# Optimization experiments

Hardware: AMD Instinct MI355X
Metric: run time of the kernel (lower is better)

The kernel has to match this reference:

```python
import jax, jax.numpy as jnp
from jax import lax
import numpy as np

T = 480000
LAYER = 32
N_HIDDEN = 2  # num_layers - 1
C1 = 4.7e-9


def _lin_init(key, out_dim, in_dim):
    kw, kb = jax.random.split(key)
    bound = 1.0 / np.sqrt(in_dim)
    W = jax.random.uniform(kw, (out_dim, in_dim), jnp.float32, -bound, bound)
    b = jax.random.uniform(kb, (out_dim,), jnp.float32, -bound, bound)
    return W, b


def setup_inputs() -> dict:
    key = jax.random.key(0)
    ks = jax.random.split(key, 8)
    v_in = jax.random.normal(ks[0], (T,), jnp.float32)
    vs_r = 10000.0 * (0.9 + 0.2 * jax.random.uniform(ks[1], (T,), jnp.float32))
    fs = jnp.full((T,), 48000.0, jnp.float32)
    W_in, b_in = _lin_init(ks[2], LAYER, 2)
    Wh, bh = [], []
    for i in range(N_HIDDEN):
        W, b = _lin_init(ks[3 + i], LAYER, LAYER)
        Wh.append(W)
        bh.append(b)
    W_h = jnp.stack(Wh)   # [N_HIDDEN, LAYER, LAYER]
    b_h = jnp.stack(bh)   # [N_HIDDEN, LAYER]
    W_out, b_out = _lin_init(ks[6], 1, LAYER)
    return {"v_in": v_in, "vs_r": vs_r, "fs": fs,
            "W_in": W_in, "b_in": b_in, "W_h": W_h, "b_h": b_h,
            "W_out": W_out, "b_out": b_out}


def reference(v_in, vs_r, fs, W_in, b_in, W_h, b_h, W_out, b_out):
    # --- per-timestep WDF port parameters (vectorized precompute) ---
    c1_r = 1.0 / (2.0 * C1 * fs)                      # [T]
    r0 = c1_r * vs_r / (c1_r + vs_r)                  # [T]
    p1_r = jnp.stack([r0, c1_r, vs_r], axis=-1)       # [T,3]
    p1_g = 1.0 / p1_r                                 # [T,3]
    P = 2.0 * p1_g / jnp.sum(p1_g, axis=-1, keepdims=True)  # [T,3]
    row0 = P.at[:, 0].add(-1.0)                       # p1[0,:] per step
    row1 = P.at[:, 1].add(-1.0)                       # p1[1,:] per step
    dp_r = r0 / 3000.0                                # [T]

    def mlp(x):  # x: [2] -> scalar, DiodePair(num_layers=3, layer_size=32)
        h = jax.nn.relu(W_in @ x + b_in)
        for i in range(W_h.shape[0]):
            h = jax.nn.relu(W_h[i] @ h + b_h[i])
        return (W_out @ h + b_out)[0]

    def step(carry, inp):
        a0, b1 = carry          # prev dp_b, prev p1_b[1]
        v, r0t, r1t, drt = inp
        a = jnp.stack([a0, b1, v])         # p1_a after updates [1],[2]
        dp_a = r0t @ a                      # p1_b[0]
        dp_b = mlp(jnp.stack([dp_a, drt]))
        a2 = jnp.stack([dp_b, b1, v])      # p1_a with [0] = dp_b
        b1n = r1t @ a2                      # p1_b[1]
        return (dp_b, b1n), 0.5 * (dp_a + dp_b)

    z = jnp.zeros((), jnp.float32)
    _, out = lax.scan(step, (z, z), (v_in, row0, row1, dp_r))
    return out
```

## Files before the change

kernel.cpp:

```cpp
#include <hip/hip_runtime.h>
#include <hip/hip_bf16.h>

#define C1_CONST 4.7e-9f
#define CHUNK 5
#define WARM  10
#define CPW   32

typedef _Float16 f16;
typedef unsigned int u32;
typedef f16   f16x8  __attribute__((ext_vector_type(8)));
typedef u32   u32x4  __attribute__((ext_vector_type(4)));
typedef float f32x16 __attribute__((ext_vector_type(16)));

#define MFMA(A, B, C) __builtin_amdgcn_mfma_f32_32x32x16_f16((A), (B), (C), 0, 0, 0)

__device__ __forceinline__ u32 packp(float x0, float x1) {
    return __builtin_bit_cast(u32, __builtin_amdgcn_cvt_pkrtz(x0, x1));
}

__global__ __launch_bounds__(64, 2) void scan_kernel(
    const float* __restrict__ v_in, const float* __restrict__ vs_r,
    const float* __restrict__ fs,
    const float* __restrict__ W_in, const float* __restrict__ b_in,
    const float* __restrict__ W_h,  const float* __restrict__ b_h,
    const float* __restrict__ W_out, const float* __restrict__ b_out,
    float* __restrict__ out, int T) {
    const int lane = threadIdx.x & 63;
    const int c    = lane & 31;
    const int h    = lane >> 5;
    const int xaddr = (lane ^ 32) << 2;

    auto xr32 = [&](float v) {
        return __int_as_float(__builtin_amdgcn_ds_bpermute(xaddr, __float_as_int(v)));
    };

    f16x8 AA0, AA1, AB0, AB1;
#pragma unroll
    for (int jj = 0; jj < 8; ++jj) {
        int k0 = (jj & 3) + 4 * h + 8 * (jj >> 2);
        int k1 = k0 + 16;
        AA0[jj] = (f16)W_h[c * 32 + k0];
        AA1[jj] = (f16)W_h[c * 32 + k1];
        AB0[jj] = (f16)W_h[1024 + c * 32 + k0];
        AB1[jj] = (f16)W_h[1024 + c * 32 + k1];
    }

    f32x16 bAf, bBf;
    float wo_r[16];
#pragma unroll
    for (int r = 0; r < 16; ++r) {
        int row = (r & 3) + 8 * (r >> 2) + 4 * h;
        bAf[r] = b_h[row];
        bBf[r] = b_h[32 + row];
        wo_r[r] = W_out[row];
    }
    const float bo = b_out[0];

    float wi0c[16], wi1c[16], bic[16];
#pragma unroll
    for (int s = 0; s < 2; ++s)
#pragma unroll
        for (int jj = 0; jj < 8; ++jj) {
            int k = (jj & 3) + 4 * h + 8 * (jj >> 2) + 16 * s;
            wi0c[s * 8 + jj] = W_in[2 * k];
            wi1c[s * 8 + jj] = W_in[2 * k + 1];
            bic[s * 8 + jj]  = b_in[k];
        }

    const int cg = blockIdx.x * CPW + c;
    const int ts = cg * CHUNK;

    auto load_pre = [&](int tt, float& P1, float& pv, float& dr) {
        int tc = min(max(tt, 0), T - 1);
        float f  = fs[tc];
        float vr = vs_r[tc];
        float vv = v_in[tc];
        float g1 = (2.0f * C1_CONST) * f;
        float g2 = __builtin_amdgcn_rcpf(vr);
        float inv = __builtin_amdgcn_rcpf(g1 + g2);
        P1 = g1 * inv;
        pv = g2 * inv * vv;
        dr = inv * (1.0f / 3000.0f);
    };

    float b1 = 0.0f;
    float P1, pv, dr;
    load_pre(ts - WARM, P1, pv, dr);

    for (int j = -WARM; j < CHUNK; ++j) {
        const int t = ts + j;
        float nP1, npv, ndr;
        load_pre(t + 1, nP1, npv, ndr);

        const float dp_a = fmaf(P1, b1, pv);

        float hv[16];
#pragma unroll
        for (int u = 0; u < 16; ++u)
            hv[u] = fmaxf(fmaf(wi0c[u], dp_a, fmaf(wi1c[u], dr, bic[u])), 0.0f);

        f16x8 B0 = __builtin_bit_cast(f16x8, (u32x4){
            packp(hv[0], hv[1]), packp(hv[2], hv[3]),
            packp(hv[4], hv[5]), packp(hv[6], hv[7])});
        f16x8 B1 = __builtin_bit_cast(f16x8, (u32x4){
            packp(hv[8], hv[9]), packp(hv[10], hv[11]),
            packp(hv[12], hv[13]), packp(hv[14], hv[15])});

        f32x16 acc = MFMA(AA0, B0, bAf);
        acc = MFMA(AA1, B1, acc);

        float v[16];
#pragma unroll
        for (int r = 0; r < 16; ++r)
            v[r] = fmaxf(acc[r], 0.0f);

        B0 = __builtin_bit_cast(f16x8, (u32x4){
            packp(v[0], v[1]), packp(v[2], v[3]),
            packp(v[4], v[5]), packp(v[6], v[7])});
        B1 = __builtin_bit_cast(f16x8, (u32x4){
            packp(v[8], v[9]), packp(v[10], v[11]),
            packp(v[12], v[13]), packp(v[14], v[15])});

        acc = MFMA(AB0, B0, bBf);
        acc = MFMA(AB1, B1, acc);

        float p0 = 0.f, p1 = 0.f, p2 = 0.f, p3 = 0.f;
#pragma unroll
        for (int r = 0; r < 16; r += 4) {
            p0 = fmaf(wo_r[r],     fmaxf(acc[r],     0.0f), p0);
            p1 = fmaf(wo_r[r + 1], fmaxf(acc[r + 1], 0.0f), p1);
            p2 = fmaf(wo_r[r + 2], fmaxf(acc[r + 2], 0.0f), p2);
            p3 = fmaf(wo_r[r + 3], fmaxf(acc[r + 3], 0.0f), p3);
        }
        float pd = (p0 + p1) + (p2 + p3);
        const float dp_b = pd + xr32(pd) + bo;

        const float sum = dp_a + dp_b;
        if (j >= 0) {
            if (lane < 32 && t < T) out[t] = 0.5f * sum;
        }
        b1 = sum - b1;
        if (t < 0) b1 = 0.0f;

        P1 = nP1; pv = npv; dr = ndr;
    }
}

extern "C" void kernel_launch(void* const* d_in, const int* in_sizes, int n_in,
                              void* d_out, int out_size, void* d_ws, size_t ws_size,
                              hipStream_t stream) {
    const float* v_in  = (const float*)d_in[0];
    const float* vs_r  = (const float*)d_in[1];
    const float* fs    = (const float*)d_in[2];
    const float* W_in  = (const float*)d_in[3];
    const float* b_in  = (const float*)d_in[4];
    const float* W_h   = (const float*)d_in[5];
    const float* b_h   = (const float*)d_in[6];
    const float* W_out = (const float*)d_in[7];
    const float* b_out = (const float*)d_in[8];
    float* out = (float*)d_out;

    const int T = in_sizes[0];
    const int nChunks = (T + CHUNK - 1) / CHUNK;
    const int nWaves  = (nChunks + CPW - 1) / CPW;

    scan_kernel<<<nWaves, 64, 0, stream>>>(
        v_in, vs_r, fs, W_in, b_in, W_h, b_h, W_out, b_out, out, T);
}
```

Measured before the change: 90.08 us.

## Move input layer onto MFMA with split-f16 inputs and use permlane32 swap

Measured after the change: 89.65 us. About the same (-0.5%).

```diff
diff --git a/kernel.cpp b/kernel.cpp
--- a/kernel.cpp
+++ b/kernel.cpp
@@ -8,6 +8,7 @@
 
 typedef _Float16 f16;
 typedef unsigned int u32;
+typedef f16   f16x2  __attribute__((ext_vector_type(2)));
 typedef f16   f16x8  __attribute__((ext_vector_type(8)));
 typedef u32   u32x4  __attribute__((ext_vector_type(4)));
 typedef float f32x16 __attribute__((ext_vector_type(16)));
@@ -18,7 +19,8 @@
     return __builtin_bit_cast(u32, __builtin_amdgcn_cvt_pkrtz(x0, x1));
 }
 
-__global__ __launch_bounds__(64, 2) void scan_kernel(
+__global__ __attribute__((amdgpu_flat_work_group_size(64, 64), amdgpu_waves_per_eu(2, 3)))
+void scan_kernel(
     const float* __restrict__ v_in, const float* __restrict__ vs_r,
     const float* __restrict__ fs,
     const float* __restrict__ W_in, const float* __restrict__ b_in,
@@ -28,11 +30,6 @@
     const int lane = threadIdx.x & 63;
     const int c    = lane & 31;
     const int h    = lane >> 5;
-    const int xaddr = (lane ^ 32) << 2;
-
-    auto xr32 = [&](float v) {
-        return __int_as_float(__builtin_amdgcn_ds_bpermute(xaddr, __float_as_int(v)));
-    };
 
     f16x8 AA0, AA1, AB0, AB1;
 #pragma unroll
@@ -45,27 +42,30 @@
         AB1[jj] = (f16)W_h[1024 + c * 32 + k1];
     }
 
-    f32x16 bAf, bBf;
+    f16x8 AIN;
+#pragma unroll
+    for (int jj = 0; jj < 8; ++jj) AIN[jj] = (f16)0.0f;
+    if (h == 0) {
+        f16 w0 = (f16)W_in[2 * c];
+        f16 w1 = (f16)W_in[2 * c + 1];
+        AIN[0] = w0;
+        AIN[1] = w1;
+        AIN[2] = w0;
+        AIN[3] = w1;
+    }
+
+    f32x16 bINf, bAf, bBf;
     float wo_r[16];
 #pragma unroll
     for (int r = 0; r < 16; ++r) {
         int row = (r & 3) + 8 * (r >> 2) + 4 * h;
-        bAf[r] = b_h[row];
-        bBf[r] = b_h[32 + row];
+        bINf[r] = b_in[row];
+        bAf[r]  = b_h[row];
+        bBf[r]  = b_h[32 + row];
         wo_r[r] = W_out[row];
     }
     const float bo = b_out[0];
-
-    float wi0c[16], wi1c[16], bic[16];
-#pragma unroll
-    for (int s = 0; s < 2; ++s)
-#pragma unroll
-        for (int jj = 0; jj < 8; ++jj) {
-            int k = (jj & 3) + 4 * h + 8 * (jj >> 2) + 16 * s;
-            wi0c[s * 8 + jj] = W_in[2 * k];
-            wi1c[s * 8 + jj] = W_in[2 * k + 1];
-            bic[s * 8 + jj]  = b_in[k];
-        }
+    const u32 hm   = h ? 0u : 0xFFFFFFFFu;
 
     const int cg = blockIdx.x * CPW + c;
     const int ts = cg * CHUNK;
@@ -94,32 +94,38 @@
 
         const float dp_a = fmaf(P1, b1, pv);
 
-        float hv[16];
+        u32 w0 = packp(dp_a, dr);
+        f16x2 hi2 = __builtin_bit_cast(f16x2, w0);
+        u32 w1 = packp(dp_a - (float)hi2[0], dr - (float)hi2[1]);
+        f16x8 BX = __builtin_bit_cast(f16x8, (u32x4){w0 & hm, w1 & hm, 0u, 0u});
+        f32x16 acc = MFMA(AIN, BX, bINf);
+
+        float v0[16];
 #pragma unroll
-        for (int u = 0; u < 16; ++u)
-            hv[u] = fmaxf(fmaf(wi0c[u], dp_a, fmaf(wi1c[u], dr, bic[u])), 0.0f);
+        for (int r = 0; r < 16; ++r)
+            v0[r] = fmaxf(acc[r], 0.0f);
 
         f16x8 B0 = __builtin_bit_cast(f16x8, (u32x4){
-            packp(hv[0], hv[1]), packp(hv[2], hv[3]),
-            packp(hv[4], hv[5]), packp(hv[6], hv[7])});
+            packp(v0[0], v0[1]), packp(v0[2], v0[3]),
+            packp(v0[4], v0[5]), packp(v0[6], v0[7])});
         f16x8 B1 = __builtin_bit_cast(f16x8, (u32x4){
-            packp(hv[8], hv[9]), packp(hv[10], hv[11]),
-            packp(hv[12], hv[13]), packp(hv[14], hv[15])});
+            packp(v0[8], v0[9]), packp(v0[10], v0[11]),
+            packp(v0[12], v0[13]), packp(v0[14], v0[15])});
 
-        f32x16 acc = MFMA(AA0, B0, bAf);
+        acc = MFMA(AA0, B0, bAf);
         acc = MFMA(AA1, B1, acc);
 
-        float v[16];
+        float v1[16];
 #pragma unroll
         for (int r = 0; r < 16; ++r)
-            v[r] = fmaxf(acc[r], 0.0f);
+            v1[r] = fmaxf(acc[r], 0.0f);
 
         B0 = __builtin_bit_cast(f16x8, (u32x4){
-            packp(v[0], v[1]), packp(v[2], v[3]),
-            packp(v[4], v[5]), packp(v[6], v[7])});
+            packp(v1[0], v1[1]), packp(v1[2], v1[3]),
+            packp(v1[4], v1[5]), packp(v1[6], v1[7])});
         B1 = __builtin_bit_cast(f16x8, (u32x4){
-            packp(v[8], v[9]), packp(v[10], v[11]),
-            packp(v[12], v[13]), packp(v[14], v[15])});
+            packp(v1[8], v1[9]), packp(v1[10], v1[11]),
+            packp(v1[12], v1[13]), packp(v1[14], v1[15])});
 
         acc = MFMA(AB0, B0, bBf);
         acc = MFMA(AB1, B1, acc);
@@ -133,7 +139,10 @@
             p3 = fmaf(wo_r[r + 3], fmaxf(acc[r + 3], 0.0f), p3);
         }
         float pd = (p0 + p1) + (p2 + p3);
-        const float dp_b = pd + xr32(pd) + bo;
+
+        float pa = pd, pb = pd;
+        asm("v_permlane32_swap_b32 %0, %1" : "+v"(pa), "+v"(pb));
+        const float dp_b = pa + pb + bo;
 
         const float sum = dp_a + dp_b;
         if (j >= 0) {
```
